# Kernel tuning notes

Hardware: AMD Instinct MI355X
Metric: run time of the kernel (lower is better)

## Reference

```python
import jax, jax.numpy as jnp
import numpy as np

N_NODES = 100000
N_EDGES = 1600000
IN_CH, HID_CH, OUT_CH = 128, 128, 64


def _spmm(row, col, val, x, n):
    # COO sparse @ dense: out[r] += val_e * x[col_e]
    gathered = val[:, None] * x[col]  # [E, d]
    return jax.ops.segment_sum(gathered, row, num_segments=n)


def setup_inputs() -> dict:
    key = jax.random.key(0)
    ks = jax.random.split(key, 8)
    x = jax.random.normal(ks[0], (N_NODES, IN_CH), dtype=jnp.float32)
    adj_row = jax.random.randint(ks[1], (N_EDGES,), 0, N_NODES)
    adj_col = jax.random.randint(ks[2], (N_EDGES,), 0, N_NODES)
    adj_val = jax.random.uniform(ks[3], (N_EDGES,), dtype=jnp.float32)
    w1 = jax.random.normal(ks[4], (IN_CH, HID_CH), dtype=jnp.float32) * (1.0 / np.sqrt(IN_CH))
    b1 = jax.random.normal(ks[5], (HID_CH,), dtype=jnp.float32) * 0.01
    w2 = jax.random.normal(ks[6], (HID_CH, OUT_CH), dtype=jnp.float32) * (1.0 / np.sqrt(HID_CH))
    b2 = jax.random.normal(ks[7], (OUT_CH,), dtype=jnp.float32) * 0.01
    return {"x": x, "adj_row": adj_row, "adj_col": adj_col, "adj_val": adj_val,
            "w1": w1, "b1": b1, "w2": w2, "b2": b2}


def reference(x, adj_row, adj_col, adj_val, w1, b1, w2, b2):
    n = x.shape[0]
    # layer 1: spmm -> linear -> relu
    h = _spmm(adj_row, adj_col, adj_val, x, n)
    h = jax.nn.relu(h @ w1 + b1)
    # layer 2: spmm -> linear
    h = _spmm(adj_row, adj_col, adj_val, h, n)
    return h @ w2 + b2
```

## Files before the change

kernel.cpp:

```cpp
#include <hip/hip_runtime.h>


typedef __bf16 v8bf __attribute__((ext_vector_type(8)));
typedef float  v4f  __attribute__((ext_vector_type(4)));
typedef unsigned v2u __attribute__((ext_vector_type(2)));

#define AS1 __attribute__((address_space(1)))
#define AS3 __attribute__((address_space(3)))

#define MAXB 800

__device__ __forceinline__ unsigned short f2bf(float f) {
    unsigned u = __float_as_uint(f);
    unsigned r = u + 0x7fffu + ((u >> 16) & 1u);
    return (unsigned short)(r >> 16);
}

__device__ __forceinline__ unsigned ldsaddr(const void* p) {
    return (unsigned)(unsigned long long)(const AS3 char*)p;
}

__device__ __forceinline__ v2u tr16(unsigned a) {
    v2u d;
    asm volatile("ds_read_b64_tr_b16 %0, %1" : "=v"(d) : "v"(a));
    return d;
}

__global__ __launch_bounds__(256) void hist_prep(const int* __restrict__ arow,
                                                 int* __restrict__ counts, int E, int B,
                                                 const float* __restrict__ w1,
                                                 const float* __restrict__ w2,
                                                 unsigned short* __restrict__ w1T,
                                                 unsigned short* __restrict__ w2T,
                                                 int* __restrict__ rowptr,
                                                 int2* __restrict__ epkS, int N) {
    const int tid = threadIdx.x;
    int gi = blockIdx.x * 256 + tid;
    if (gi < 16384) {
        int n = gi >> 7, k = gi & 127;
        w1T[gi] = f2bf(w1[k * 128 + n]);
    } else if (gi < 24576) {
        int i2 = gi - 16384;
        int n = i2 >> 7, k = i2 & 127;
        w2T[i2] = f2bf(w2[k * 64 + n]);
    } else if (gi < 24576 + 32) {
        epkS[E + (gi - 24576)] = make_int2(0, 0);
    } else if (gi == 24576 + 32) {
        rowptr[N] = E;
    }
    __shared__ int lh[MAXB];
    for (int i = tid; i < B; i += 256) lh[i] = 0;
    __syncthreads();
    const int base = blockIdx.x * 4096;
#pragma unroll
    for (int j = 0; j < 16; ++j) {
        int i = base + j * 256 + tid;
        if (i < E) atomicAdd(&lh[arow[i] >> 7], 1);
    }
    __syncthreads();
    for (int i = tid; i < B; i += 256) {
        int c = lh[i];
        if (c) atomicAdd(&counts[i], c);
    }
}

__global__ __launch_bounds__(256) void scan_s(const int* __restrict__ counts,
                                              int* __restrict__ boff,
                                              int* __restrict__ gcursor, int B, int E) {
    __shared__ int lds[256];
    const int t = threadIdx.x;
    const int b0 = t * 4;
    int v[4];
    int s = 0;
#pragma unroll
    for (int j = 0; j < 4; ++j) {
        v[j] = (b0 + j < B) ? counts[b0 + j] : 0;
        s += v[j];
    }
    lds[t] = s;
    __syncthreads();
    for (int off = 1; off < 256; off <<= 1) {
        int tmp = 0;
        if (t >= off) tmp = lds[t - off];
        __syncthreads();
        if (t >= off) lds[t] += tmp;
        __syncthreads();
    }
    int run = (t > 0) ? lds[t - 1] : 0;
#pragma unroll
    for (int j = 0; j < 4; ++j) {
        if (b0 + j < B) {
            boff[b0 + j] = run;
            gcursor[b0 + j] = run;
        }
        run += v[j];
    }
    if (t == 255) boff[B] = E;
}

__global__ __launch_bounds__(256) void partition_k(const int* __restrict__ arow,
                                                   const int* __restrict__ acol,
                                                   const float* __restrict__ aval,
                                                   int* __restrict__ gcursor,
                                                   int2* __restrict__ epk, int E, int B) {
    __shared__ int2 ldata[4096];
    __shared__ int ldest[4096];
    __shared__ int lhist[MAXB];
    __shared__ int lscan[MAXB];
    __shared__ int ldelta[MAXB];
    __shared__ int lcur[MAXB];
    __shared__ int stmp[256];
    const int tid = threadIdx.x;
    const int base = blockIdx.x * 4096;
    const int cnt = min(4096, E - base);

    for (int i = tid; i < MAXB; i += 256) {
        lhist[i] = 0;
        lcur[i] = 0;
    }
    __syncthreads();

    int rr[16];
#pragma unroll
    for (int j = 0; j < 16; ++j) {
        int i = base + j * 256 + tid;
        rr[j] = (i < E) ? arow[i] : -1;
        if (rr[j] >= 0) atomicAdd(&lhist[rr[j] >> 7], 1);
    }
    __syncthreads();

    const int b0 = tid * 4;
    int v[4];
    int s = 0;
#pragma unroll
    for (int j = 0; j < 4; ++j) {
        v[j] = (b0 + j < MAXB) ? lhist[b0 + j] : 0;
        s += v[j];
    }
    stmp[tid] = s;
    __syncthreads();
    for (int off = 1; off < 256; off <<= 1) {
        int tmp = 0;
        if (tid >= off) tmp = stmp[tid - off];
        __syncthreads();
        if (tid >= off) stmp[tid] += tmp;
        __syncthreads();
    }
    int run = (tid > 0) ? stmp[tid - 1] : 0;
#pragma unroll
    for (int j = 0; j < 4; ++j) {
        if (b0 + j < MAXB) lscan[b0 + j] = run;
        run += v[j];
    }
    __syncthreads();

    for (int b = tid; b < B; b += 256) {
        int c = lhist[b];
        if (c) ldelta[b] = atomicAdd(&gcursor[b], c) - lscan[b];
    }
    __syncthreads();

#pragma unroll
    for (int j = 0; j < 16; ++j) {
        int i = base + j * 256 + tid;
        if (i < E) {
            int r = rr[j];
            int b = r >> 7;
            int lp = atomicAdd(&lcur[b], 1);
            int slot = lscan[b] + lp;
            int pk = acol[i] | ((r & 127) << 17);
            ldata[slot] = make_int2(pk, __float_as_int(aval[i]));
            ldest[slot] = ldelta[b] + slot;
        }
    }
    __syncthreads();

    for (int s2 = tid; s2 < cnt; s2 += 256) epk[ldest[s2]] = ldata[s2];
}

template <int NC, bool AF32>
__device__ __forceinline__ void gemm_body(const void* __restrict__ A,
                                          const unsigned short* __restrict__ wT,
                                          unsigned short* __restrict__ y, int M,
                                          int bid, char* smem) {
    constexpr int KP = 136;
    constexpr int NT = NC / 16;
    unsigned short* wl = (unsigned short*)smem;
    const int tid = threadIdx.x;
    for (int idx = tid; idx < NC * 16; idx += 256) {
        int n = idx >> 4, kc = idx & 15;
        *(uint4*)&wl[n * KP + kc * 8] = *(const uint4*)&wT[n * 128 + kc * 8];
    }
    __syncthreads();

    const int wave = tid >> 6;
    const int lane = tid & 63;
    const int m = lane & 15;
    const int q = lane >> 4;
    const int rowbase = bid * 64 + wave * 16;
    const int rowc = min(rowbase + m, M - 1);

    v4f acc[NT] = {};
    union LU { uint4 qv; v8bf b; };

#pragma unroll
    for (int ks = 0; ks < 4; ++ks) {
        const int k0 = ks * 32 + q * 8;
        v8bf a;
        if (AF32) {
            const float* Ap = (const float*)A + (size_t)rowc * 128 + k0;
            float4 f0 = *(const float4*)Ap;
            float4 f1 = *(const float4*)(Ap + 4);
            union { unsigned short s[8]; v8bf b; } cv;
            cv.s[0] = f2bf(f0.x); cv.s[1] = f2bf(f0.y);
            cv.s[2] = f2bf(f0.z); cv.s[3] = f2bf(f0.w);
            cv.s[4] = f2bf(f1.x); cv.s[5] = f2bf(f1.y);
            cv.s[6] = f2bf(f1.z); cv.s[7] = f2bf(f1.w);
            a = cv.b;
        } else {
            LU lu;
            lu.qv = *(const uint4*)((const unsigned short*)A + (size_t)rowc * 128 + k0);
            a = lu.b;
        }
#pragma unroll
        for (int nt = 0; nt < NT; ++nt) {
            v8bf b = *(const v8bf*)&wl[(nt * 16 + m) * KP + k0];
            acc[nt] = __builtin_amdgcn_mfma_f32_16x16x32_bf16(a, b, acc[nt], 0, 0, 0);
        }
    }
#pragma unroll
    for (int nt = 0; nt < NT; ++nt) {
#pragma unroll
        for (int r = 0; r < 4; ++r) {
            int orow = rowbase + q * 4 + r;
            if (orow < M) y[(size_t)orow * NC + nt * 16 + m] = f2bf(acc[nt][r]);
        }
    }
}

__global__ __launch_bounds__(256) void sort_gemm1(const int* __restrict__ boff,
                                                  const int2* __restrict__ epk,
                                                  int2* __restrict__ epkS,
                                                  int* __restrict__ rowptr, int N, int B,
                                                  const float* __restrict__ x,
                                                  const unsigned short* __restrict__ w1T,
                                                  unsigned short* __restrict__ y1b) {
    __shared__ __align__(16) char smem[34816];
    const int tid = threadIdx.x;
    if (blockIdx.x >= B) {
        gemm_body<128, true>(x, w1T, y1b, N, blockIdx.x - B, smem);
        return;
    }
    int2* sorted = (int2*)smem;
    int*  sc     = (int*)(smem + 32768);
    int*  lcur   = (int*)(smem + 32768 + 512);
    const int b = blockIdx.x;
    const int s = boff[b], e = boff[b + 1];
    const int cnt = min(e - s, 4096);
    if (tid < 128) sc[tid] = 0;
    __syncthreads();
    for (int i = s + tid; i < e; i += 256) {
        int rl = (epk[i].x >> 17) & 127;
        atomicAdd(&sc[rl], 1);
    }
    __syncthreads();
    int hv = (tid < 128) ? sc[tid] : 0;
    for (int off = 1; off < 128; off <<= 1) {
        int add = 0;
        if (tid < 128 && tid >= off) add = sc[tid - off];
        __syncthreads();
        if (tid < 128 && tid >= off) sc[tid] += add;
        __syncthreads();
    }
    if (tid < 128) {
        int ex = sc[tid] - hv;
        lcur[tid] = ex;
        int r = b * 128 + tid;
        if (r < N) rowptr[r] = s + ex;
    }
    __syncthreads();
    for (int i = s + tid; i < e; i += 256) {
        int2 p = epk[i];
        int rl = (p.x >> 17) & 127;
        int slot = atomicAdd(&lcur[rl], 1);
        if (slot < 4096) sorted[slot] = p;
    }
    __syncthreads();
    for (int i = tid; i < cnt; i += 256) epkS[s + i] = sorted[i];
}

template <int NT>
__device__ __forceinline__ void issue_dma(const unsigned short* __restrict__ yb,
                                          int colg, int lane, char* NB) {
    const char* gp = (const char*)yb + ((size_t)(unsigned)colg << (NT == 8 ? 8 : 7)) +
                     ((lane & 1) << 4);
#pragma unroll
    for (int t = 0; t < NT; ++t)
        __builtin_amdgcn_global_load_lds((const AS1 unsigned*)(gp + t * 32),
                                         (AS3 unsigned*)(NB + t * 1024), 16, 0, 0);
}

template <int NT>
__device__ __forceinline__ void spmm_mfma_pipe(int si, int ei, int E,
                                               const int2* __restrict__ ep,
                                               const unsigned short* __restrict__ yb,
                                               char* NB0, char* NB1, char* AT0, char* AT1,
                                               int lane, v4f* acc) {
    const int m = lane & 15, q = lane >> 4;
    const int l31 = lane & 31;
    const unsigned trBo = (unsigned)(q * 256 + m * 8);
    const int nch = (ei - si + 31) >> 5;
    if (nch <= 0) return;
    int2 peA = ep[min(si + l31, E + 31)];
    {
        int colg0 = __shfl(peA.x & 0x1FFFF, lane >> 1);
        issue_dma<NT>(yb, colg0, lane, NB0);
    }
    int2 peB = ep[min(si + 32 + l31, E + 31)];
#pragma unroll 1
    for (int c = 0; c < nch; ++c) {
        char* curN = (c & 1) ? NB1 : NB0;
        char* nxtN = (c & 1) ? NB0 : NB1;
        const int cb = si + c * 32;
        const bool more = (c + 1 < nch);
        int2 peC = ep[min(cb + 64 + l31, E + 31)];
        __builtin_amdgcn_sched_barrier(0);
        if (more) {
            int colgN = __shfl(peB.x & 0x1FFFF, lane >> 1);
            issue_dma<NT>(yb, colgN, lane, nxtN);
        }
        __builtin_amdgcn_sched_barrier(0);
        const uint4 z4 = make_uint4(0u, 0u, 0u, 0u);
        *(uint4*)(AT0 + lane * 16) = z4;
        *(uint4*)(AT1 + lane * 16) = z4;
        if (lane < 32 && cb + l31 < ei) {
            const float v = __int_as_float(peA.y);
            const unsigned short vh = f2bf(v);
            const float vhf = __uint_as_float((unsigned)vh << 16);
            const unsigned short vl = f2bf(v - vhf);
            const int rl4 = (peA.x >> 17) & 15;
            *(unsigned short*)(AT0 + rl4 * 64 + l31 * 2) = vh;
            *(unsigned short*)(AT1 + rl4 * 64 + l31 * 2) = vl;
        }
        if (more) {
            if constexpr (NT == 8) asm volatile("s_waitcnt vmcnt(9)" ::: "memory");
            else                   asm volatile("s_waitcnt vmcnt(5)" ::: "memory");
        } else {
            asm volatile("s_waitcnt vmcnt(0)" ::: "memory");
        }
        __builtin_amdgcn_sched_barrier(0);
        const unsigned trB = ldsaddr(curN) + trBo;
        v2u tr0[NT], tr1[NT];
#pragma unroll
        for (int h = 0; h < NT; ++h) {
            tr0[h] = tr16(trB + h * 1024);
            tr1[h] = tr16(trB + h * 1024 + 128);
        }
        const v8bf avh = *(const v8bf*)(AT0 + m * 64 + q * 16);
        const v8bf avl = *(const v8bf*)(AT1 + m * 64 + q * 16);
        asm volatile("s_waitcnt lgkmcnt(0)" ::: "memory");
        __builtin_amdgcn_sched_barrier(0);
#pragma unroll
        for (int h = 0; h < NT; ++h) {
            union { unsigned u[4]; v8bf b; } bu;
            bu.u[0] = tr0[h][0]; bu.u[1] = tr0[h][1];
            bu.u[2] = tr1[h][0]; bu.u[3] = tr1[h][1];
            acc[h] = __builtin_amdgcn_mfma_f32_16x16x32_bf16(avh, bu.b, acc[h], 0, 0, 0);
            acc[h] = __builtin_amdgcn_mfma_f32_16x16x32_bf16(avl, bu.b, acc[h], 0, 0, 0);
        }
        peA = peB;
        peB = peC;
    }
}

__global__ __launch_bounds__(128) void spmm_gemm2(const int* __restrict__ rowptr,
                                                  const int2* __restrict__ ep,
                                                  const unsigned short* __restrict__ y1b,
                                                  const float* __restrict__ b1,
                                                  const unsigned short* __restrict__ w2T,
                                                  unsigned short* __restrict__ y2b,
                                                  int N, int E) {
    constexpr int KP = 136;
    __shared__ __align__(1024) char smem[36864];
    const int tid = threadIdx.x;
    const int wave = tid >> 6, lane = tid & 63;
    char* W = smem + wave * 18432;
    const int rowbase = blockIdx.x * 32;
    const int r0 = rowbase + wave * 16;
    const int si = __builtin_amdgcn_readfirstlane(rowptr[min(r0, N)]);
    const int ei = __builtin_amdgcn_readfirstlane(rowptr[min(r0 + 16, N)]);
    const int m = lane & 15, q = lane >> 4;

    v4f acc[8] = {};
    spmm_mfma_pipe<8>(si, ei, E, ep, y1b, W, W + 8192, W + 16384, W + 17408, lane, acc);
    __syncthreads();
    unsigned short* h1 = (unsigned short*)smem;
#pragma unroll
    for (int h = 0; h < 8; ++h) {
        const float bv = b1[h * 16 + m];
#pragma unroll
        for (int r = 0; r < 4; ++r) {
            const float f = fmaxf(acc[h][r] + bv, 0.f);
            h1[(wave * 16 + q * 4 + r) * KP + h * 16 + m] = f2bf(f);
        }
    }
    __syncthreads();

    v4f acc2[4] = {};
#pragma unroll
    for (int ks = 0; ks < 4; ++ks) {
        const int k0 = ks * 32 + q * 8;
        v8bf av = *(const v8bf*)&h1[(wave * 16 + m) * KP + k0];
#pragma unroll
        for (int nt = 0; nt < 4; ++nt) {
            v8bf b = *(const v8bf*)&w2T[(nt * 16 + m) * 128 + k0];
            acc2[nt] = __builtin_amdgcn_mfma_f32_16x16x32_bf16(av, b, acc2[nt], 0, 0, 0);
        }
    }
#pragma unroll
    for (int nt = 0; nt < 4; ++nt) {
#pragma unroll
        for (int r = 0; r < 4; ++r) {
            int orow = rowbase + wave * 16 + q * 4 + r;
            if (orow < N) y2b[(size_t)orow * 64 + nt * 16 + m] = f2bf(acc2[nt][r]);
        }
    }
}

__global__ __launch_bounds__(256) void spmm64(const int* __restrict__ rowptr,
                                              const int2* __restrict__ ep,
                                              const unsigned short* __restrict__ yb,
                                              const float* __restrict__ bias,
                                              float* __restrict__ outp, int N, int E) {
    __shared__ __align__(1024) char smem[40960];
    const int tid = threadIdx.x;
    const int wave = tid >> 6, lane = tid & 63;
    char* W = smem + wave * 10240;
    const int r0 = blockIdx.x * 64 + wave * 16;
    const int si = __builtin_amdgcn_readfirstlane(rowptr[min(r0, N)]);
    const int ei = __builtin_amdgcn_readfirstlane(rowptr[min(r0 + 16, N)]);
    const int m = lane & 15, q = lane >> 4;

    v4f acc[4] = {};
    spmm_mfma_pipe<4>(si, ei, E, ep, yb, W, W + 4096, W + 8192, W + 9216, lane, acc);

#pragma unroll
    for (int h = 0; h < 4; ++h) {
        const float bv = bias[h * 16 + m];
#pragma unroll
        for (int r = 0; r < 4; ++r) {
            const int orow = r0 + q * 4 + r;
            if (orow < N) outp[(size_t)orow * 64 + h * 16 + m] = acc[h][r] + bv;
        }
    }
}

extern "C" void kernel_launch(void* const* d_in, const int* in_sizes, int n_in,
                              void* d_out, int out_size, void* d_ws, size_t ws_size,
                              hipStream_t stream) {
    const float* x    = (const float*)d_in[0];
    const int*   arow = (const int*)d_in[1];
    const int*   acol = (const int*)d_in[2];
    const float* aval = (const float*)d_in[3];
    const float* w1   = (const float*)d_in[4];
    const float* b1   = (const float*)d_in[5];
    const float* w2   = (const float*)d_in[6];
    const float* b2   = (const float*)d_in[7];
    float*       out  = (float*)d_out;

    const int N = in_sizes[0] / 128;
    const int E = in_sizes[1];
    const int B = (N + 127) >> 7;

    char* p = (char*)d_ws;
    auto alloc = [&](size_t bytes) {
        char* r = p;
        p += (bytes + 255) & ~(size_t)255;
        return r;
    };
    int*            counts  = (int*)alloc((size_t)MAXB * 4);
    int*            boff    = (int*)alloc((size_t)(MAXB + 1) * 4);
    int*            gcursor = (int*)alloc((size_t)MAXB * 4);
    int*            rowptr  = (int*)alloc((size_t)(N + 1) * 4);
    int2*           epkS    = (int2*)alloc((size_t)(E + 32) * 8);
    unsigned short* w1T     = (unsigned short*)alloc(128 * 128 * 2);
    unsigned short* w2T     = (unsigned short*)alloc(64 * 128 * 2);
    unsigned short* y1b     = (unsigned short*)alloc((size_t)N * 128 * 2);
    int2*           epk     = (int2*)alloc((size_t)E * 8);
    unsigned short* y2b     = (unsigned short*)alloc((size_t)N * 64 * 2);

    const int gemm_blocks = (N + 63) / 64;
    const int pb = (E + 4095) / 4096;

    hipMemsetAsync(counts, 0, (size_t)MAXB * 4, stream);
    hist_prep<<<pb, 256, 0, stream>>>(arow, counts, E, B, w1, w2, w1T, w2T,
                                      rowptr, epkS, N);
    scan_s<<<1, 256, 0, stream>>>(counts, boff, gcursor, B, E);
    partition_k<<<pb, 256, 0, stream>>>(arow, acol, aval, gcursor, epk, E, B);
    sort_gemm1<<<B + gemm_blocks, 256, 0, stream>>>(boff, epk, epkS, rowptr, N, B,
                                                    x, w1T, y1b);
    const int sg2_blocks = (N + 31) / 32;
    spmm_gemm2<<<sg2_blocks, 128, 0, stream>>>(rowptr, epkS, y1b, b1, w2T, y2b, N, E);
    spmm64<<<gemm_blocks, 256, 0, stream>>>(rowptr, epkS, y2b, b2, out, N, E);
}
```

Before: 277.3 us.

## Replace LDS-DMA gathers with register-prefetched loads and staged edge lists

The sparse-dense gather pipeline no longer uses global_load_lds DMA into double-buffered LDS. Each wave now stages up to 512 edges of its row segment into LDS and gathers neighbour feature rows into registers one chunk ahead, ping-ponging between two register sets. Each chunk is then written into a single LDS buffer before the transpose reads and MFMA accumulation. This aims to cut per-chunk edge-list global loads and shuffles and to overlap gathers through registers, at the cost of more VGPRs and an extra LDS write per chunk.

```diff
diff --git a/kernel.cpp b/kernel.cpp
--- a/kernel.cpp
+++ b/kernel.cpp
@@ -5,7 +5,6 @@
 typedef float  v4f  __attribute__((ext_vector_type(4)));
 typedef unsigned v2u __attribute__((ext_vector_type(2)));
 
-#define AS1 __attribute__((address_space(1)))
 #define AS3 __attribute__((address_space(3)))
 
 #define MAXB 800
@@ -290,86 +289,105 @@
 }
 
 template <int NT>
-__device__ __forceinline__ void issue_dma(const unsigned short* __restrict__ yb,
-                                          int colg, int lane, char* NB) {
-    const char* gp = (const char*)yb + ((size_t)(unsigned)colg << (NT == 8 ? 8 : 7)) +
-                     ((lane & 1) << 4);
-#pragma unroll
-    for (int t = 0; t < NT; ++t)
-        __builtin_amdgcn_global_load_lds((const AS1 unsigned*)(gp + t * 32),
-                                         (AS3 unsigned*)(NB + t * 1024), 16, 0, 0);
+__device__ __forceinline__ void chunk_body(int c, int seg, int segE,
+                                           const char* __restrict__ ybB,
+                                           char* NB, char* AT0, char* AT1,
+                                           const char* epL,
+                                           int lane, int er, int oc, unsigned wro,
+                                           unsigned trBo, v4f* acc,
+                                           uint4* cur, uint4* nxt) {
+    constexpr int EPR = (NT == 8) ? 4 : 8;
+    constexpr int RB = NT * 32;
+    const int m = lane & 15, q = lane >> 4;
+    const int l31 = lane & 31;
+#pragma unroll
+    for (int i = 0; i < NT; ++i) {
+        const int2 pc = *(const int2*)(epL + ((c + 1) * 32 + i * EPR + er) * 8);
+        nxt[i] = *(const uint4*)(ybB + (size_t)(unsigned)(pc.x & 0x1FFFF) * RB + oc * 16);
+    }
+    __builtin_amdgcn_sched_barrier(0);
+    const uint4 z4 = make_uint4(0u, 0u, 0u, 0u);
+    *(uint4*)(AT0 + lane * 16) = z4;
+    *(uint4*)(AT1 + lane * 16) = z4;
+    if (lane < 32 && seg + c * 32 + l31 < segE) {
+        const int2 pv = *(const int2*)(epL + (c * 32 + l31) * 8);
+        const float v = __int_as_float(pv.y);
+        const unsigned short vh = f2bf(v);
+        const float vhf = __uint_as_float((unsigned)vh << 16);
+        const unsigned short vl = f2bf(v - vhf);
+        const int rl4 = (pv.x >> 17) & 15;
+        *(unsigned short*)(AT0 + rl4 * 64 + l31 * 2) = vh;
+        *(unsigned short*)(AT1 + rl4 * 64 + l31 * 2) = vl;
+    }
+    if constexpr (NT == 8) asm volatile("s_waitcnt vmcnt(8)" ::: "memory");
+    else                   asm volatile("s_waitcnt vmcnt(4)" ::: "memory");
+    __builtin_amdgcn_sched_barrier(0);
+#pragma unroll
+    for (int i = 0; i < NT; ++i)
+        *(uint4*)(NB + wro + (unsigned)(i * EPR + er) * 32) = cur[i];
+    __builtin_amdgcn_sched_barrier(0);
+    const unsigned trB = ldsaddr(NB) + trBo;
+    v2u tr0[NT], tr1[NT];
+#pragma unroll
+    for (int h = 0; h < NT; ++h) {
+        tr0[h] = tr16(trB + h * 1024);
+        tr1[h] = tr16(trB + h * 1024 + 128);
+    }
+    const v8bf avh = *(const v8bf*)(AT0 + m * 64 + q * 16);
+    const v8bf avl = *(const v8bf*)(AT1 + m * 64 + q * 16);
+    asm volatile("s_waitcnt lgkmcnt(0)" ::: "memory");
+    __builtin_amdgcn_sched_barrier(0);
+#pragma unroll
+    for (int h = 0; h < NT; ++h) {
+        union { unsigned u[4]; v8bf b; } bu;
+        bu.u[0] = tr0[h][0]; bu.u[1] = tr0[h][1];
+        bu.u[2] = tr1[h][0]; bu.u[3] = tr1[h][1];
+        acc[h] = __builtin_amdgcn_mfma_f32_16x16x32_bf16(avh, bu.b, acc[h], 0, 0, 0);
+        acc[h] = __builtin_amdgcn_mfma_f32_16x16x32_bf16(avl, bu.b, acc[h], 0, 0, 0);
+    }
 }
 
 template <int NT>
 __device__ __forceinline__ void spmm_mfma_pipe(int si, int ei, int E,
                                                const int2* __restrict__ ep,
                                                const unsigned short* __restrict__ yb,
-                                               char* NB0, char* NB1, char* AT0, char* AT1,
+                                               char* NB, char* AT0, char* AT1, char* epL,
                                                int lane, v4f* acc) {
-    const int m = lane & 15, q = lane >> 4;
-    const int l31 = lane & 31;
+    constexpr int GSH = (NT == 8) ? 4 : 3;
+    constexpr int EPR = 64 >> GSH;
+    constexpr int RB = NT * 32;
+    const int er = lane >> GSH;
+    const int oc = lane & ((1 << GSH) - 1);
+    const unsigned wro = (unsigned)((oc >> 1) * 1024 + (oc & 1) * 16);
+    const int q = lane >> 4, m = lane & 15;
     const unsigned trBo = (unsigned)(q * 256 + m * 8);
-    const int nch = (ei - si + 31) >> 5;
-    if (nch <= 0) return;
-    int2 peA = ep[min(si + l31, E + 31)];
-    {
-        int colg0 = __shfl(peA.x & 0x1FFFF, lane >> 1);
-        issue_dma<NT>(yb, colg0, lane, NB0);
-    }
-    int2 peB = ep[min(si + 32 + l31, E + 31)];
+    const char* ybB = (const char*)yb;
+
+    for (int seg = si; seg < ei; seg += 512) {
+        const int segE = min(seg + 512, ei);
+#pragma unroll
+        for (int j = 0; j < 9; ++j) {
+            const int idx = j * 64 + lane;
+            if (idx < 544) {
+                const int2 t = ep[min(seg + idx, E + 31)];
+                *(int2*)(epL + idx * 8) = t;
+            }
+        }
+        const int nch = (segE - seg + 31) >> 5;
+        const int nchE = (nch + 1) & ~1;
+        uint4 gX[NT], gY[NT];
+#pragma unroll
+        for (int i = 0; i < NT; ++i) {
+            const int2 pc = *(const int2*)(epL + (i * EPR + er) * 8);
+            gX[i] = *(const uint4*)(ybB + (size_t)(unsigned)(pc.x & 0x1FFFF) * RB + oc * 16);
+        }
 #pragma unroll 1
-    for (int c = 0; c < nch; ++c) {
-        char* curN = (c & 1) ? NB1 : NB0;
-        char* nxtN = (c & 1) ? NB0 : NB1;
-        const int cb = si + c * 32;
-        const bool more = (c + 1 < nch);
-        int2 peC = ep[min(cb + 64 + l31, E + 31)];
-        __builtin_amdgcn_sched_barrier(0);
-        if (more) {
-            int colgN = __shfl(peB.x & 0x1FFFF, lane >> 1);
-            issue_dma<NT>(yb, colgN, lane, nxtN);
-        }
-        __builtin_amdgcn_sched_barrier(0);
-        const uint4 z4 = make_uint4(0u, 0u, 0u, 0u);
-        *(uint4*)(AT0 + lane * 16) = z4;
-        *(uint4*)(AT1 + lane * 16) = z4;
-        if (lane < 32 && cb + l31 < ei) {
-            const float v = __int_as_float(peA.y);
-            const unsigned short vh = f2bf(v);
-            const float vhf = __uint_as_float((unsigned)vh << 16);
-            const unsigned short vl = f2bf(v - vhf);
-            const int rl4 = (peA.x >> 17) & 15;
-            *(unsigned short*)(AT0 + rl4 * 64 + l31 * 2) = vh;
-            *(unsigned short*)(AT1 + rl4 * 64 + l31 * 2) = vl;
-        }
-        if (more) {
-            if constexpr (NT == 8) asm volatile("s_waitcnt vmcnt(9)" ::: "memory");
-            else                   asm volatile("s_waitcnt vmcnt(5)" ::: "memory");
-        } else {
-            asm volatile("s_waitcnt vmcnt(0)" ::: "memory");
-        }
-        __builtin_amdgcn_sched_barrier(0);
-        const unsigned trB = ldsaddr(curN) + trBo;
-        v2u tr0[NT], tr1[NT];
-#pragma unroll
-        for (int h = 0; h < NT; ++h) {
-            tr0[h] = tr16(trB + h * 1024);
-            tr1[h] = tr16(trB + h * 1024 + 128);
-        }
-        const v8bf avh = *(const v8bf*)(AT0 + m * 64 + q * 16);
-        const v8bf avl = *(const v8bf*)(AT1 + m * 64 + q * 16);
-        asm volatile("s_waitcnt lgkmcnt(0)" ::: "memory");
-        __builtin_amdgcn_sched_barrier(0);
-#pragma unroll
-        for (int h = 0; h < NT; ++h) {
-            union { unsigned u[4]; v8bf b; } bu;
-            bu.u[0] = tr0[h][0]; bu.u[1] = tr0[h][1];
-            bu.u[2] = tr1[h][0]; bu.u[3] = tr1[h][1];
-            acc[h] = __builtin_amdgcn_mfma_f32_16x16x32_bf16(avh, bu.b, acc[h], 0, 0, 0);
-            acc[h] = __builtin_amdgcn_mfma_f32_16x16x32_bf16(avl, bu.b, acc[h], 0, 0, 0);
-        }
-        peA = peB;
-        peB = peC;
+        for (int c = 0; c < nchE; c += 2) {
+            chunk_body<NT>(c, seg, segE, ybB, NB, AT0, AT1, epL, lane, er, oc,
+                           wro, trBo, acc, gX, gY);
+            chunk_body<NT>(c + 1, seg, segE, ybB, NB, AT0, AT1, epL, lane, er, oc,
+                           wro, trBo, acc, gY, gX);
+        }
     }
 }
 
@@ -381,10 +399,10 @@
                                                   unsigned short* __restrict__ y2b,
                                                   int N, int E) {
     constexpr int KP = 136;
-    __shared__ __align__(1024) char smem[36864];
+    __shared__ __align__(1024) char smem[30720];
     const int tid = threadIdx.x;
     const int wave = tid >> 6, lane = tid & 63;
-    char* W = smem + wave * 18432;
+    char* W = smem + wave * 15360;
     const int rowbase = blockIdx.x * 32;
     const int r0 = rowbase + wave * 16;
     const int si = __builtin_amdgcn_readfirstlane(rowptr[min(r0, N)]);
@@ -392,7 +410,7 @@
     const int m = lane & 15, q = lane >> 4;
 
     v4f acc[8] = {};
-    spmm_mfma_pipe<8>(si, ei, E, ep, y1b, W, W + 8192, W + 16384, W + 17408, lane, acc);
+    spmm_mfma_pipe<8>(si, ei, E, ep, y1b, W, W + 8192, W + 9216, W + 10240, lane, acc);
     __syncthreads();
     unsigned short* h1 = (unsigned short*)smem;
 #pragma unroll
@@ -432,17 +450,17 @@
                                               const unsigned short* __restrict__ yb,
                                               const float* __restrict__ bias,
                                               float* __restrict__ outp, int N, int E) {
-    __shared__ __align__(1024) char smem[40960];
+    __shared__ __align__(1024) char smem[45056];
     const int tid = threadIdx.x;
     const int wave = tid >> 6, lane = tid & 63;
-    char* W = smem + wave * 10240;
+    char* W = smem + wave * 11264;
     const int r0 = blockIdx.x * 64 + wave * 16;
     const int si = __builtin_amdgcn_readfirstlane(rowptr[min(r0, N)]);
     const int ei = __builtin_amdgcn_readfirstlane(rowptr[min(r0 + 16, N)]);
     const int m = lane & 15, q = lane >> 4;
 
     v4f acc[4] = {};
-    spmm_mfma_pipe<4>(si, ei, E, ep, yb, W, W + 4096, W + 8192, W + 9216, lane, acc);
+    spmm_mfma_pipe<4>(si, ei, E, ep, yb, W, W + 4096, W + 5120, W + 6144, lane, acc);
 
 #pragma unroll
     for (int h = 0; h < 4; ++h) {
```

Result: slower. 467.4 us (+68.5%).
